# Kernel optimization log

Measured on AMD Instinct MI355X. Metric: run time of the kernel, lower is better.

## Reference

```python
import jax, jax.numpy as jnp
import numpy as np

N, D_FEAT, D, H, L = 2048, 128, 256, 8, 2
DH = D // H
E = 65536
NUM_EDGE_TYPES = 8
MAX_DIST = 10
MAX_DEGREE = 512
D_FF = 4 * D
D_OUT = 128
EPS = 1e-5


def _layernorm(x, g, b):
    mu = jnp.mean(x, axis=-1, keepdims=True)
    var = jnp.mean(jnp.square(x - mu), axis=-1, keepdims=True)
    return (x - mu) * jax.lax.rsqrt(var + EPS) * g + b


def setup_inputs() -> dict:
    key = jax.random.key(0)
    ks = jax.random.split(key, 32)
    inp = {
        "x": jax.random.normal(ks[0], (N, D_FEAT), dtype=jnp.float32),
        "edge_index": jax.random.randint(ks[1], (2, E), 0, N),
        "edge_types": jax.random.randint(ks[2], (E,), 0, NUM_EDGE_TYPES),
        "pos_encoding": jax.random.uniform(ks[3], (N, N), dtype=jnp.float32),
    }
    def xavier(k, shape):
        fan_in, fan_out = shape[0], shape[1]
        lim = float(np.sqrt(6.0 / (fan_in + fan_out)))
        return jax.random.uniform(k, shape, jnp.float32, -lim, lim)
    inp["W_emb"] = xavier(ks[4], (D_FEAT, D)); inp["b_emb"] = jnp.zeros((D,), jnp.float32)
    # stacked per-layer params, stored as [in, out] so y = x @ W + b
    inp["Wq"] = jnp.stack([xavier(jax.random.fold_in(ks[5], l), (D, D)) for l in range(L)])
    inp["Wk"] = jnp.stack([xavier(jax.random.fold_in(ks[6], l), (D, D)) for l in range(L)])
    inp["Wv"] = jnp.stack([xavier(jax.random.fold_in(ks[7], l), (D, D)) for l in range(L)])
    inp["Wo"] = jnp.stack([xavier(jax.random.fold_in(ks[8], l), (D, D)) for l in range(L)])
    for nm in ("bq", "bk", "bv", "bo"):
        inp[nm] = jnp.zeros((L, D), jnp.float32)
    inp["spd_table"] = 0.02 * jax.random.normal(ks[9], (L, MAX_DIST + 1, H), dtype=jnp.float32)
    inp["edge_table"] = 0.02 * jax.random.normal(ks[10], (L, NUM_EDGE_TYPES, H), dtype=jnp.float32)
    inp["din_emb"] = 0.02 * jax.random.normal(ks[11], (L, MAX_DEGREE + 1, D), dtype=jnp.float32)
    inp["dout_emb"] = 0.02 * jax.random.normal(ks[12], (L, MAX_DEGREE + 1, D), dtype=jnp.float32)
    inp["ln1_g"] = jnp.ones((L, D), jnp.float32); inp["ln1_b"] = jnp.zeros((L, D), jnp.float32)
    inp["ln2_g"] = jnp.ones((L, D), jnp.float32); inp["ln2_b"] = jnp.zeros((L, D), jnp.float32)
    inp["W1"] = jnp.stack([xavier(jax.random.fold_in(ks[13], l), (D, D_FF)) for l in range(L)])
    inp["b1"] = jnp.zeros((L, D_FF), jnp.float32)
    inp["W2"] = jnp.stack([xavier(jax.random.fold_in(ks[14], l), (D_FF, D)) for l in range(L)])
    inp["b2"] = jnp.zeros((L, D), jnp.float32)
    inp["W_out"] = xavier(ks[15], (D, D_OUT)); inp["b_out"] = jnp.zeros((D_OUT,), jnp.float32)
    return inp


def _forward(x, edge_index, edge_types, pos_encoding,
             W_emb, b_emb, Wq, bq, Wk, bk, Wv, bv, Wo, bo,
             spd_table, edge_table, din_emb, dout_emb,
             ln1_g, ln1_b, ln2_g, ln2_b, W1, b1, W2, b2, W_out, b_out):
    src, dst = edge_index[0], edge_index[1]
    ones = jnp.ones((E,), jnp.int32)
    deg_out = jnp.clip(jax.ops.segment_sum(ones, src, num_segments=N), 0, MAX_DEGREE)
    deg_in = jnp.clip(jax.ops.segment_sum(ones, dst, num_segments=N), 0, MAX_DEGREE)
    # SPD bucket matrix [N, N] (int), shared across layers
    spd_bucket = jnp.clip(pos_encoding[:, :N] * MAX_DIST + 0.5, 0, MAX_DIST).astype(jnp.int32)

    h = x @ W_emb + b_emb  # node embedding; dropout=0 (eval)
    scale = 1.0 / np.sqrt(DH)
    for l in range(L):
        # centrality encoding
        h = h + din_emb[l][deg_in] + dout_emb[l][deg_out]
        xn = _layernorm(h, ln1_g[l], ln1_b[l])
        q = (xn @ Wq[l] + bq[l]).reshape(N, H, DH).transpose(1, 0, 2)  # [H,N,DH]
        k = (xn @ Wk[l] + bk[l]).reshape(N, H, DH).transpose(1, 0, 2)
        v = (xn @ Wv[l] + bv[l]).reshape(N, H, DH).transpose(1, 0, 2)
        # attention bias [H, N, N]: SPD table gather + per-edge scatter-add
        bias = spd_table[l][spd_bucket].transpose(2, 0, 1)
        e_bias = edge_table[l][edge_types]  # [E, H]
        bias = bias.at[:, src, dst].add(e_bias.T)
        scores = jnp.einsum('hnd,hmd->hnm', q, k) * scale + bias
        attn = jax.nn.softmax(scores, axis=-1)
        attn_out = jnp.einsum('hnm,hmd->hnd', attn, v).transpose(1, 0, 2).reshape(N, D)
        h = h + attn_out @ Wo[l] + bo[l]
        y = _layernorm(h, ln2_g[l], ln2_b[l])
        y = jax.nn.gelu(y @ W1[l] + b1[l], approximate=False) @ W2[l] + b2[l]
        h = h + y
    return h @ W_out + b_out


def reference(x, edge_index, edge_types, pos_encoding,
              W_emb, b_emb, Wq, bq, Wk, bk, Wv, bv, Wo, bo,
              spd_table, edge_table, din_emb, dout_emb,
              ln1_g, ln1_b, ln2_g, ln2_b, W1, b1, W2, b2, W_out, b_out):
    return _forward(x, edge_index, edge_types, pos_encoding,
                    W_emb, b_emb, Wq, bq, Wk, bk, Wv, bv, Wo, bo,
                    spd_table, edge_table, din_emb, dout_emb,
                    ln1_g, ln1_b, ln2_g, ln2_b, W1, b1, W2, b2, W_out, b_out)
```

## Files before the change

kernel.cpp:

```cpp
#include <hip/hip_runtime.h>
#include <math.h>

#define N_NODES 2048
#define D_MODEL 256
#define D_FEAT 128
#define NHEAD 8
#define DH 32
#define NLAYER 2
#define NEDGE 65536
#define D_FF 1024
#define D_OUT 128
#define MAXDEG 512
#define JSPLIT 4

typedef __attribute__((ext_vector_type(8))) short short8;
typedef __attribute__((ext_vector_type(4))) float f32x4;
typedef __attribute__((ext_vector_type(4))) unsigned short u16x4;

__device__ __forceinline__ unsigned short f2bf(float f) {
    unsigned u = __float_as_uint(f);
    unsigned r = (u + 0x7FFFu + ((u >> 16) & 1u)) >> 16;
    return (unsigned short)r;
}

template <int CTRL>
__device__ __forceinline__ float dpp_ror(float x) {
    return __int_as_float(__builtin_amdgcn_update_dpp(0, __float_as_int(x), CTRL, 0xf, 0xf, false));
}

__device__ __forceinline__ void wt_tile(const float* __restrict__ W, unsigned short* __restrict__ Wt,
                                        int K, int Nc, int n0, int k0, int tid,
                                        unsigned short (*tile)[33]) {
    int r = tid >> 3, cg = (tid & 7) * 4;
    float4 w4 = *(const float4*)&W[(size_t)(k0 + r) * Nc + n0 + cg];
    tile[r][cg + 0] = f2bf(w4.x); tile[r][cg + 1] = f2bf(w4.y);
    tile[r][cg + 2] = f2bf(w4.z); tile[r][cg + 3] = f2bf(w4.w);
    __syncthreads();
    int c = tid >> 3, rg = (tid & 7) * 4;
    u16x4 o;
    #pragma unroll
    for (int j = 0; j < 4; j++) o[j] = tile[rg + j][c];
    *(u16x4*)&Wt[(size_t)(n0 + c) * K + k0 + rg] = o;
}

__global__ void mega_prep_kernel(const float* __restrict__ pos, unsigned char* __restrict__ bucket,
                                 unsigned* __restrict__ hist, int* __restrict__ deg_out,
                                 int* __restrict__ deg_in, unsigned* __restrict__ gcursor,
                                 const float* __restrict__ Wq, const float* __restrict__ Wk,
                                 const float* __restrict__ Wv, const float* __restrict__ Wo,
                                 const float* __restrict__ W1, const float* __restrict__ W2,
                                 const float* __restrict__ W_emb, const float* __restrict__ W_out,
                                 const float* __restrict__ bq, const float* __restrict__ bk,
                                 const float* __restrict__ bv,
                                 unsigned short* __restrict__ qkvt, unsigned short* __restrict__ wot,
                                 unsigned short* __restrict__ w1t, unsigned short* __restrict__ w2t,
                                 unsigned short* __restrict__ wembt, unsigned short* __restrict__ woutt,
                                 float* __restrict__ bqkv) {
    __shared__ unsigned short tile[32][33];
    int b = blockIdx.x, tid = threadIdx.x;
    if (b < 4096) {
        int i = b * 256 + tid;
        float4 p = *(const float4*)&pos[(size_t)i * 4];
        unsigned b0 = (unsigned)fminf(fmaxf(p.x * 10.f + 0.5f, 0.f), 10.f);
        unsigned b1 = (unsigned)fminf(fmaxf(p.y * 10.f + 0.5f, 0.f), 10.f);
        unsigned b2 = (unsigned)fminf(fmaxf(p.z * 10.f + 0.5f, 0.f), 10.f);
        unsigned b3 = (unsigned)fminf(fmaxf(p.w * 10.f + 0.5f, 0.f), 10.f);
        ((unsigned*)bucket)[i] = b0 | (b1 << 8) | (b2 << 16) | (b3 << 24);
        if (b < 64) {
            #pragma unroll
            for (int k = 0; k < 4; k++) hist[b * 1024 + k * 256 + tid] = 0;
        } else if (b == 64) {
            #pragma unroll
            for (int k = 0; k < 8; k++) deg_out[k * 256 + tid] = 0;
            #pragma unroll
            for (int k = 0; k < 8; k++) deg_in[k * 256 + tid] = 0;
            if (tid == 0) *gcursor = 0;
        }
        return;
    }
    int bb = b - 4096;
    if (bb < 512) {
        int z = bb >> 6, t = bb & 63;
        int l = z >> 2, which = z & 3;
        const float* W = (which == 0 ? Wq : which == 1 ? Wk : which == 2 ? Wv : Wo) + (size_t)l * 65536;
        unsigned short* dst = (which < 3) ? qkvt + (size_t)l * 196608 + which * 65536
                                          : wot + (size_t)l * 65536;
        wt_tile(W, dst, 256, 256, (t & 7) * 32, (t >> 3) * 32, tid, tile);
    } else if (bb < 1024) {
        int b2 = bb - 512, l = b2 >> 8, t = b2 & 255;
        wt_tile(W1 + (size_t)l * D_MODEL * D_FF, w1t + (size_t)l * D_MODEL * D_FF,
                D_MODEL, D_FF, (t & 31) * 32, (t >> 5) * 32, tid, tile);
    } else if (bb < 1536) {
        int b3 = bb - 1024, l = b3 >> 8, t = b3 & 255;
        wt_tile(W2 + (size_t)l * D_FF * D_MODEL, w2t + (size_t)l * D_FF * D_MODEL,
                D_FF, D_MODEL, (t & 7) * 32, (t >> 3) * 32, tid, tile);
    } else if (bb < 1568) {
        int b4 = bb - 1536;
        wt_tile(W_emb, wembt, D_FEAT, D_MODEL, (b4 & 7) * 32, (b4 >> 3) * 32, tid, tile);
    } else if (bb < 1600) {
        int b5 = bb - 1568;
        wt_tile(W_out, woutt, D_MODEL, D_OUT, (b5 & 3) * 32, (b5 >> 2) * 32, tid, tile);
    } else {
        int i = (bb - 1600) * 256 + tid;
        if (i < NLAYER * 768) {
            int l = i / 768, j = i % 768;
            const float* src = j < 256 ? bq : j < 512 ? bk : bv;
            bqkv[i] = src[l * 256 + (j & 255)];
        }
    }
}

__global__ void degree_hist_kernel(const int* __restrict__ ei,
                                   int* __restrict__ deg_out, int* __restrict__ deg_in,
                                   unsigned* __restrict__ hist) {
    int e = blockIdx.x * 256 + threadIdx.x;
    if (e < NEDGE) {
        int src = ei[e], dst = ei[NEDGE + e];
        atomicAdd(&deg_out[src], 1);
        atomicAdd(&deg_in[dst], 1);
        atomicAdd(&hist[(src >> 6) * 2048 + dst], 1);
    }
}

__global__ void edge_alloc_kernel(const unsigned* __restrict__ hist,
                                  unsigned* __restrict__ offsets, unsigned* __restrict__ cursor,
                                  unsigned* __restrict__ gend, unsigned* __restrict__ gcursor) {
    int g = blockIdx.x;
    int t = threadIdx.x;
    unsigned v = hist[g * 64 + t];
    unsigned inc = v;
    #pragma unroll
    for (int off = 1; off < 64; off <<= 1) {
        unsigned u = __shfl_up(inc, off);
        if (t >= off) inc += u;
    }
    unsigned total = __shfl(inc, 63);
    unsigned base = 0;
    if (t == 63) base = atomicAdd(gcursor, total);
    base = __shfl(base, 63);
    unsigned o = base + inc - v;
    offsets[g * 64 + t] = o;
    cursor[g * 64 + t] = o;
    if (t == 63) gend[g] = base + total;
}

__global__ void edge_scatter_kernel(const int* __restrict__ ei, const int* __restrict__ etypes,
                                    unsigned* __restrict__ cursor, unsigned* __restrict__ packed) {
    int e = blockIdx.x * 256 + threadIdx.x;
    if (e < NEDGE) {
        int src = ei[e], dst = ei[NEDGE + e];
        int key = (src >> 6) * 2048 + dst;
        unsigned pos = atomicAdd(&cursor[key], 1);
        packed[pos] = (unsigned)dst | ((unsigned)(src & 63) << 11) | ((unsigned)etypes[e] << 17);
    }
}

__global__ void centrality_ln_kernel(float* __restrict__ h,
                                     const float* __restrict__ din_l,
                                     const float* __restrict__ dout_l,
                                     const int* __restrict__ deg_in,
                                     const int* __restrict__ deg_out,
                                     const float* __restrict__ g,
                                     const float* __restrict__ b,
                                     unsigned short* __restrict__ y) {
    int row = blockIdx.x;
    int tid = threadIdx.x;
    int di = min(max(deg_in[row], 0), MAXDEG);
    int dn = min(max(deg_out[row], 0), MAXDEG);
    float v = h[row * D_MODEL + tid] + din_l[di * D_MODEL + tid] + dout_l[dn * D_MODEL + tid];
    h[row * D_MODEL + tid] = v;
    __shared__ float red[256];
    red[tid] = v; __syncthreads();
    for (int s = 128; s > 0; s >>= 1) { if (tid < s) red[tid] += red[tid + s]; __syncthreads(); }
    float mu = red[0] * (1.0f / D_MODEL);
    __syncthreads();
    float d = v - mu;
    red[tid] = d * d; __syncthreads();
    for (int s = 128; s > 0; s >>= 1) { if (tid < s) red[tid] += red[tid + s]; __syncthreads(); }
    float rstd = rsqrtf(red[0] * (1.0f / D_MODEL) + 1e-5f);
    y[row * D_MODEL + tid] = f2bf(d * rstd * g[tid] + b[tid]);
}

__global__ void layernorm_kernel(const float* __restrict__ x,
                                 const float* __restrict__ g,
                                 const float* __restrict__ b,
                                 unsigned short* __restrict__ y) {
    int row = blockIdx.x;
    int tid = threadIdx.x;
    float v = x[row * D_MODEL + tid];
    __shared__ float red[256];
    red[tid] = v; __syncthreads();
    for (int s = 128; s > 0; s >>= 1) { if (tid < s) red[tid] += red[tid + s]; __syncthreads(); }
    float mu = red[0] * (1.0f / D_MODEL);
    __syncthreads();
    float d = v - mu;
    red[tid] = d * d; __syncthreads();
    for (int s = 128; s > 0; s >>= 1) { if (tid < s) red[tid] += red[tid + s]; __syncthreads(); }
    float rstd = rsqrtf(red[0] * (1.0f / D_MODEL) + 1e-5f);
    y[row * D_MODEL + tid] = f2bf(d * rstd * g[tid] + b[tid]);
}

template <int ACT, bool RESID, bool OUTBF16, bool AFP32>
__global__ void gemm_mfma_kernel(const void* __restrict__ Av,
                                 const unsigned short* __restrict__ Wt,
                                 const float* __restrict__ bias,
                                 float* __restrict__ C, unsigned short* __restrict__ Cb,
                                 int Nc, int K) {
    __shared__ __align__(16) unsigned short As[32][72];
    __shared__ __align__(16) unsigned short Bs[64][72];
    const unsigned short* A16 = (const unsigned short*)Av;
    const float* A32 = (const float*)Av;
    int tid = threadIdx.x;
    int m0 = blockIdx.y * 32, n0 = blockIdx.x * 64;
    int w = tid >> 6, lane = tid & 63;
    int rg = (w & 1) * 16, cg = (w >> 1) * 32;
    int m = lane & 15, quad = lane >> 4;
    f32x4 acc[2] = {{0.f, 0.f, 0.f, 0.f}, {0.f, 0.f, 0.f, 0.f}};
    int ar = tid >> 3, ac = (tid & 7) * 8;
    uint4 ra; float4 fa0, fa1; uint4 rb0, rb1;
    if (AFP32) {
        fa0 = *(const float4*)&A32[(size_t)(m0 + ar) * K + ac];
        fa1 = *(const float4*)&A32[(size_t)(m0 + ar) * K + ac + 4];
    } else {
        ra = *(const uint4*)&A16[(size_t)(m0 + ar) * K + ac];
    }
    rb0 = *(const uint4*)&Wt[(size_t)(n0 + ar) * K + ac];
    rb1 = *(const uint4*)&Wt[(size_t)(n0 + 32 + ar) * K + ac];
    for (int k0 = 0; k0 < K; k0 += 64) {
        if (AFP32) {
            u16x4 t0 = {f2bf(fa0.x), f2bf(fa0.y), f2bf(fa0.z), f2bf(fa0.w)};
            u16x4 t1 = {f2bf(fa1.x), f2bf(fa1.y), f2bf(fa1.z), f2bf(fa1.w)};
            *(u16x4*)&As[ar][ac] = t0;
            *(u16x4*)&As[ar][ac + 4] = t1;
        } else {
            *(uint4*)&As[ar][ac] = ra;
        }
        *(uint4*)&Bs[ar][ac] = rb0;
        *(uint4*)&Bs[ar + 32][ac] = rb1;
        __syncthreads();
        int kn = k0 + 64;
        if (kn < K) {
            if (AFP32) {
                fa0 = *(const float4*)&A32[(size_t)(m0 + ar) * K + kn + ac];
                fa1 = *(const float4*)&A32[(size_t)(m0 + ar) * K + kn + ac + 4];
            } else {
                ra = *(const uint4*)&A16[(size_t)(m0 + ar) * K + kn + ac];
            }
            rb0 = *(const uint4*)&Wt[(size_t)(n0 + ar) * K + kn + ac];
            rb1 = *(const uint4*)&Wt[(size_t)(n0 + 32 + ar) * K + kn + ac];
        }
        #pragma unroll
        for (int ks = 0; ks < 2; ks++) {
            short8 a = *(const short8*)&As[rg + m][ks * 32 + quad * 8];
            #pragma unroll
            for (int t = 0; t < 2; t++) {
                short8 b = *(const short8*)&Bs[cg + t * 16 + m][ks * 32 + quad * 8];
                acc[t] = __builtin_amdgcn_mfma_f32_16x16x32_bf16(a, b, acc[t], 0, 0, 0);
            }
        }
        __syncthreads();
    }
    #pragma unroll
    for (int t = 0; t < 2; t++) {
        #pragma unroll
        for (int reg = 0; reg < 4; reg++) {
            int row = m0 + rg + quad * 4 + reg;
            int col = n0 + cg + t * 16 + m;
            float val = acc[t][reg] + bias[col];
            if (ACT == 1) val = val * 0.5f * (1.0f + erff(val * 0.7071067811865476f));
            size_t idx = (size_t)row * Nc + col;
            if (RESID) val += C[idx];
            if (OUTBF16) Cb[idx] = f2bf(val);
            else C[idx] = val;
        }
    }
}

__global__ void gemm_oproj_kernel(const float* __restrict__ part_O,
                                  const float* __restrict__ l_part,
                                  const unsigned short* __restrict__ Wt,
                                  const float* __restrict__ bias,
                                  float* __restrict__ C) {
    __shared__ __align__(16) unsigned short As[32][72];
    __shared__ __align__(16) unsigned short Bs[64][72];
    int tid = threadIdx.x;
    int m0 = blockIdx.y * 32, n0 = blockIdx.x * 64;
    int w = tid >> 6, lane = tid & 63;
    int rg = (w & 1) * 16, cg = (w >> 1) * 32;
    int m = lane & 15, quad = lane >> 4;
    f32x4 acc[2] = {{0.f, 0.f, 0.f, 0.f}, {0.f, 0.f, 0.f, 0.f}};
    int ar = tid >> 3, ac = (tid & 7) * 8;
    int row = m0 + ar;
    for (int k0 = 0; k0 < D_MODEL; k0 += 64) {
        int col = k0 + ac;
        int hh = col >> 5;
        float L = 0.f;
        float o[8] = {0.f, 0.f, 0.f, 0.f, 0.f, 0.f, 0.f, 0.f};
        #pragma unroll
        for (int js = 0; js < JSPLIT; js++) {
            L += l_part[((size_t)js * NHEAD + hh) * N_NODES + row];
            const float* pp = &part_O[((size_t)js * N_NODES + row) * D_MODEL + col];
            float4 p0 = *(const float4*)pp;
            float4 p1 = *(const float4*)(pp + 4);
            o[0] += p0.x; o[1] += p0.y; o[2] += p0.z; o[3] += p0.w;
            o[4] += p1.x; o[5] += p1.y; o[6] += p1.z; o[7] += p1.w;
        }
        float inv = 1.0f / L;
        u16x4 t0, t1;
        #pragma unroll
        for (int j = 0; j < 4; j++) { t0[j] = f2bf(o[j] * inv); t1[j] = f2bf(o[j + 4] * inv); }
        *(u16x4*)&As[ar][ac] = t0;
        *(u16x4*)&As[ar][ac + 4] = t1;
        *(uint4*)&Bs[ar][ac] = *(const uint4*)&Wt[(size_t)(n0 + ar) * D_MODEL + k0 + ac];
        *(uint4*)&Bs[ar + 32][ac] = *(const uint4*)&Wt[(size_t)(n0 + 32 + ar) * D_MODEL + k0 + ac];
        __syncthreads();
        #pragma unroll
        for (int ks = 0; ks < 2; ks++) {
            short8 a = *(const short8*)&As[rg + m][ks * 32 + quad * 8];
            #pragma unroll
            for (int t = 0; t < 2; t++) {
                short8 b = *(const short8*)&Bs[cg + t * 16 + m][ks * 32 + quad * 8];
                acc[t] = __builtin_amdgcn_mfma_f32_16x16x32_bf16(a, b, acc[t], 0, 0, 0);
            }
        }
        __syncthreads();
    }
    #pragma unroll
    for (int t = 0; t < 2; t++) {
        #pragma unroll
        for (int reg = 0; reg < 4; reg++) {
            int orow = m0 + rg + quad * 4 + reg;
            int ocol = n0 + cg + t * 16 + m;
            size_t idx = (size_t)orow * D_MODEL + ocol;
            C[idx] += acc[t][reg] + bias[ocol];
        }
    }
}

template <int ACT, bool VOUT>
__global__ void gemm64_kernel(const unsigned short* __restrict__ A,
                              const unsigned short* __restrict__ Wt,
                              const float* __restrict__ bias,
                              unsigned short* __restrict__ Cb,
                              unsigned short* __restrict__ vbt,
                              int Nc, int K) {
    __shared__ __align__(16) unsigned short As[64][72];
    __shared__ __align__(16) unsigned short Bs[64][72];
    int tid = threadIdx.x;
    int m0 = blockIdx.y * 64, n0 = blockIdx.x * 64;
    int w = tid >> 6, lane = tid & 63;
    int wr = (w & 1) * 32, wc = (w >> 1) * 32;
    int m = lane & 15, quad = lane >> 4;
    f32x4 acc[2][2] = {{{0.f,0.f,0.f,0.f},{0.f,0.f,0.f,0.f}},{{0.f,0.f,0.f,0.f},{0.f,0.f,0.f,0.f}}};
    int sr = tid >> 2, sg = (tid & 3) * 16;
    uint4 a0 = *(const uint4*)&A[(size_t)(m0 + sr) * K + sg];
    uint4 a1 = *(const uint4*)&A[(size_t)(m0 + sr) * K + sg + 8];
    uint4 b0 = *(const uint4*)&Wt[(size_t)(n0 + sr) * K + sg];
    uint4 b1 = *(const uint4*)&Wt[(size_t)(n0 + sr) * K + sg + 8];
    for (int k0 = 0; k0 < K; k0 += 64) {
        *(uint4*)&As[sr][sg] = a0;
        *(uint4*)&As[sr][sg + 8] = a1;
        *(uint4*)&Bs[sr][sg] = b0;
        *(uint4*)&Bs[sr][sg + 8] = b1;
        __syncthreads();
        int kn = k0 + 64;
        if (kn < K) {
            a0 = *(const uint4*)&A[(size_t)(m0 + sr) * K + kn + sg];
            a1 = *(const uint4*)&A[(size_t)(m0 + sr) * K + kn + sg + 8];
            b0 = *(const uint4*)&Wt[(size_t)(n0 + sr) * K + kn + sg];
            b1 = *(const uint4*)&Wt[(size_t)(n0 + sr) * K + kn + sg + 8];
        }
        #pragma unroll
        for (int kh = 0; kh < 2; kh++) {
            short8 x0 = *(const short8*)&As[wr + m][kh * 32 + quad * 8];
            short8 x1 = *(const short8*)&As[wr + 16 + m][kh * 32 + quad * 8];
            short8 y0 = *(const short8*)&Bs[wc + m][kh * 32 + quad * 8];
            short8 y1 = *(const short8*)&Bs[wc + 16 + m][kh * 32 + quad * 8];
            acc[0][0] = __builtin_amdgcn_mfma_f32_16x16x32_bf16(x0, y0, acc[0][0], 0, 0, 0);
            acc[0][1] = __builtin_amdgcn_mfma_f32_16x16x32_bf16(x0, y1, acc[0][1], 0, 0, 0);
            acc[1][0] = __builtin_amdgcn_mfma_f32_16x16x32_bf16(x1, y0, acc[1][0], 0, 0, 0);
            acc[1][1] = __builtin_amdgcn_mfma_f32_16x16x32_bf16(x1, y1, acc[1][1], 0, 0, 0);
        }
        __syncthreads();
    }
    if (VOUT && n0 >= 512) {
        #pragma unroll
        for (int mt = 0; mt < 2; mt++) {
            #pragma unroll
            for (int nt = 0; nt < 2; nt++) {
                int row0 = m0 + wr + mt * 16 + quad * 4;
                int col = n0 + wc + nt * 16 + m;
                float bcol = bias[col];
                u16x4 tv;
                #pragma unroll
                for (int reg = 0; reg < 4; reg++) tv[reg] = f2bf(acc[mt][nt][reg] + bcol);
                *(u16x4*)&vbt[(size_t)(col - 512) * N_NODES + row0] = tv;
            }
        }
        return;
    }
    #pragma unroll
    for (int mt = 0; mt < 2; mt++) {
        #pragma unroll
        for (int nt = 0; nt < 2; nt++) {
            #pragma unroll
            for (int reg = 0; reg < 4; reg++) {
                int row = m0 + wr + mt * 16 + quad * 4 + reg;
                int col = n0 + wc + nt * 16 + m;
                float val = acc[mt][nt][reg] + bias[col];
                if (ACT == 1) val = val * 0.5f * (1.0f + erff(val * 0.7071067811865476f));
                Cb[(size_t)row * Nc + col] = f2bf(val);
            }
        }
    }
}

__global__ __launch_bounds__(256)
void flash_attn_kernel(const unsigned short* __restrict__ qkvb,
                       const unsigned short* __restrict__ vbt,
                       const unsigned char* __restrict__ bucket,
                       const float* __restrict__ spd_l,
                       const float* __restrict__ et_l,
                       const unsigned* __restrict__ offsets,
                       const unsigned* __restrict__ gend,
                       const unsigned* __restrict__ packed,
                       float* __restrict__ part_O,
                       float* __restrict__ l_part) {
    __shared__ __align__(16) unsigned short ks[64][40];
    __shared__ __align__(16) unsigned short vs[32][72];
    __shared__ __align__(16) float ov[64][68];
    __shared__ float et[8];

    int tid = threadIdx.x;
    int rb = blockIdx.x;
    int i0 = rb * 64;
    int hh = blockIdx.y;
    int js = blockIdx.z;
    int lane = tid & 63;
    if (tid < 8) et[tid] = et_l[tid * NHEAD + hh];
    float spd_reg = spd_l[(lane < 11 ? lane : 10) * NHEAD + hh];

    int w = tid >> 6;
    int m = lane & 15, quad = lane >> 4;
    int r0 = w * 16;
    short8 aq = *(const short8*)&qkvb[(size_t)(i0 + r0 + m) * 768 + hh * DH + quad * 8];
    float l_st[4] = {0.f, 0.f, 0.f, 0.f};
    f32x4 oacc[2] = {{0.f, 0.f, 0.f, 0.f}, {0.f, 0.f, 0.f, 0.f}};
    const float scale = 0.17677669529663687f;

    int krow = tid >> 2, kcol = (tid & 3) * 8;
    int vrow = tid >> 3, vcol = (tid & 7) * 8;
    int brow = tid >> 2, bcol = (tid & 3) * 16;

    for (int jt = 0; jt < N_NODES / JSPLIT / 64; jt++) {
        int j0 = js * (N_NODES / JSPLIT) + jt * 64;
        __syncthreads();
        *(uint4*)&ks[krow][kcol] =
            *(const uint4*)&qkvb[(size_t)(j0 + krow) * 768 + 256 + hh * DH + kcol];
        *(uint4*)&vs[vrow][vcol] =
            *(const uint4*)&vbt[(size_t)(hh * DH + vrow) * N_NODES + j0 + vcol];
        {
            uint4 b16 = *(const uint4*)&bucket[(size_t)(i0 + brow) * N_NODES + j0 + bcol];
            const unsigned char* bb = (const unsigned char*)&b16;
            float fb[16];
            #pragma unroll
            for (int i = 0; i < 16; i++)
                fb[i] = __int_as_float(
                    __builtin_amdgcn_ds_bpermute(((int)bb[i]) << 2, __float_as_int(spd_reg)));
            #pragma unroll
            for (int g = 0; g < 4; g++) {
                f32x4 st = {fb[g * 4], fb[g * 4 + 1], fb[g * 4 + 2], fb[g * 4 + 3]};
                *(f32x4*)&ov[brow][bcol + g * 4] = st;
            }
        }
        __syncthreads();
        {
            unsigned key0 = (unsigned)rb * 2048 + j0;
            unsigned start = offsets[key0], end = gend[key0 >> 6];
            for (unsigned i = start + tid; i < end; i += 256) {
                unsigned p = packed[i];
                atomicAdd(&ov[(p >> 11) & 63][(p & 2047) - j0], et[(p >> 17) & 7]);
            }
        }
        __syncthreads();
        float sv[4][4];
        #pragma unroll
        for (int t = 0; t < 4; t++) {
            short8 bk8 = *(const short8*)&ks[t * 16 + m][quad * 8];
            f32x4 z = {0.f, 0.f, 0.f, 0.f};
            f32x4 sacc = __builtin_amdgcn_mfma_f32_16x16x32_bf16(aq, bk8, z, 0, 0, 0);
            #pragma unroll
            for (int r = 0; r < 4; r++)
                sv[t][r] = __expf(sacc[r] * scale + ov[r0 + quad * 4 + r][t * 16 + m]);
        }
        #pragma unroll
        for (int r = 0; r < 4; r++) {
            float ps = sv[0][r] + sv[1][r] + sv[2][r] + sv[3][r];
            ps += dpp_ror<0x121>(ps);
            ps += dpp_ror<0x122>(ps);
            ps += dpp_ror<0x124>(ps);
            ps += dpp_ror<0x128>(ps);
            l_st[r] += ps;
        }
        #pragma unroll
        for (int t = 0; t < 4; t++)
            #pragma unroll
            for (int r = 0; r < 4; r++)
                ov[r0 + quad * 4 + r][t * 16 + m] = sv[t][r];
        __builtin_amdgcn_s_waitcnt(0xC07F);
        #pragma unroll
        for (int kh = 0; kh < 2; kh++) {
            f32x4 p0 = *(const f32x4*)&ov[r0 + m][kh * 32 + quad * 8];
            f32x4 p1 = *(const f32x4*)&ov[r0 + m][kh * 32 + quad * 8 + 4];
            short8 pa;
            pa[0] = (short)f2bf(p0[0]); pa[1] = (short)f2bf(p0[1]);
            pa[2] = (short)f2bf(p0[2]); pa[3] = (short)f2bf(p0[3]);
            pa[4] = (short)f2bf(p1[0]); pa[5] = (short)f2bf(p1[1]);
            pa[6] = (short)f2bf(p1[2]); pa[7] = (short)f2bf(p1[3]);
            #pragma unroll
            for (int t = 0; t < 2; t++) {
                short8 vb = *(const short8*)&vs[t * 16 + m][kh * 32 + quad * 8];
                oacc[t] = __builtin_amdgcn_mfma_f32_16x16x32_bf16(pa, vb, oacc[t], 0, 0, 0);
            }
        }
    }
    #pragma unroll
    for (int t = 0; t < 2; t++)
        #pragma unroll
        for (int r = 0; r < 4; r++)
            part_O[((size_t)js * N_NODES + i0 + r0 + quad * 4 + r) * D_MODEL + hh * DH + t * 16 + m] =
                oacc[t][r];
    if (m == 0) {
        #pragma unroll
        for (int r = 0; r < 4; r++) {
            int row = i0 + r0 + quad * 4 + r;
            l_part[((size_t)js * NHEAD + hh) * N_NODES + row] = l_st[r];
        }
    }
}

#define WS_ALLOC(type, name, count) \
    type* name = (type*)base; base += (((size_t)(count) * sizeof(type)) + 255) & ~(size_t)255;

extern "C" void kernel_launch(void* const* d_in, const int* in_sizes, int n_in,
                              void* d_out, int out_size, void* d_ws, size_t ws_size,
                              hipStream_t stream) {
    const float* x          = (const float*)d_in[0];
    const int*   edge_index = (const int*)d_in[1];
    const int*   edge_types = (const int*)d_in[2];
    const float* pos        = (const float*)d_in[3];
    const float* W_emb      = (const float*)d_in[4];
    const float* b_emb      = (const float*)d_in[5];
    const float* Wq         = (const float*)d_in[6];
    const float* Wk         = (const float*)d_in[7];
    const float* Wv         = (const float*)d_in[8];
    const float* Wo         = (const float*)d_in[9];
    const float* bq         = (const float*)d_in[10];
    const float* bk         = (const float*)d_in[11];
    const float* bv         = (const float*)d_in[12];
    const float* bo         = (const float*)d_in[13];
    const float* spd_table  = (const float*)d_in[14];
    const float* edge_table = (const float*)d_in[15];
    const float* din_emb    = (const float*)d_in[16];
    const float* dout_emb   = (const float*)d_in[17];
    const float* ln1_g      = (const float*)d_in[18];
    const float* ln1_b      = (const float*)d_in[19];
    const float* ln2_g      = (const float*)d_in[20];
    const float* ln2_b      = (const float*)d_in[21];
    const float* W1         = (const float*)d_in[22];
    const float* b1         = (const float*)d_in[23];
    const float* W2         = (const float*)d_in[24];
    const float* b2         = (const float*)d_in[25];
    const float* W_out      = (const float*)d_in[26];
    const float* b_out      = (const float*)d_in[27];
    float* out = (float*)d_out;

    char* base = (char*)d_ws;
    WS_ALLOC(int, deg_out, N_NODES)
    WS_ALLOC(int, deg_in, N_NODES)
    WS_ALLOC(float, h, N_NODES * D_MODEL)
    WS_ALLOC(unsigned short, xb, N_NODES * D_MODEL)
    WS_ALLOC(unsigned short, qkvb, N_NODES * 768)
    WS_ALLOC(unsigned short, vbt, D_MODEL * N_NODES)
    WS_ALLOC(unsigned short, ffnb, N_NODES * D_FF)
    WS_ALLOC(unsigned char, bucket, (size_t)N_NODES * N_NODES)
    WS_ALLOC(unsigned short, qkvt, NLAYER * 768 * D_MODEL)
    WS_ALLOC(unsigned short, wot, NLAYER * D_MODEL * D_MODEL)
    WS_ALLOC(unsigned short, w1t, NLAYER * D_MODEL * D_FF)
    WS_ALLOC(unsigned short, w2t, NLAYER * D_FF * D_MODEL)
    WS_ALLOC(unsigned short, wembt, D_FEAT * D_MODEL)
    WS_ALLOC(unsigned short, woutt, D_MODEL * D_OUT)
    WS_ALLOC(float, bqkv, NLAYER * 768)
    WS_ALLOC(unsigned, hist, 65536)
    WS_ALLOC(unsigned, offsets, 65536)
    WS_ALLOC(unsigned, cursor, 65536)
    WS_ALLOC(unsigned, gend, 1024)
    WS_ALLOC(unsigned, gcursor, 1)
    WS_ALLOC(unsigned, packed, NEDGE)
    WS_ALLOC(float, part_O, (size_t)JSPLIT * N_NODES * D_MODEL)
    WS_ALLOC(float, l_part, (size_t)JSPLIT * NHEAD * N_NODES)

    mega_prep_kernel<<<5702, 256, 0, stream>>>(pos, bucket, hist, deg_out, deg_in, gcursor,
                                               Wq, Wk, Wv, Wo, W1, W2, W_emb, W_out,
                                               bq, bk, bv, qkvt, wot, w1t, w2t, wembt, woutt, bqkv);
    degree_hist_kernel<<<NEDGE / 256, 256, 0, stream>>>(edge_index, deg_out, deg_in, hist);
    edge_alloc_kernel<<<1024, 64, 0, stream>>>(hist, offsets, cursor, gend, gcursor);
    edge_scatter_kernel<<<NEDGE / 256, 256, 0, stream>>>(edge_index, edge_types, cursor, packed);

    gemm_mfma_kernel<0, false, false, true><<<dim3(D_MODEL / 64, N_NODES / 32), 256, 0, stream>>>(
        x, wembt, b_emb, h, nullptr, D_MODEL, D_FEAT);

    for (int l = 0; l < NLAYER; l++) {
        centrality_ln_kernel<<<N_NODES, 256, 0, stream>>>(
            h, din_emb + (size_t)l * (MAXDEG + 1) * D_MODEL,
            dout_emb + (size_t)l * (MAXDEG + 1) * D_MODEL, deg_in, deg_out,
            ln1_g + l * D_MODEL, ln1_b + l * D_MODEL, xb);

        gemm64_kernel<0, true><<<dim3(768 / 64, N_NODES / 64), 256, 0, stream>>>(
            xb, qkvt + (size_t)l * 768 * D_MODEL, bqkv + l * 768, qkvb, vbt, 768, D_MODEL);

        flash_attn_kernel<<<dim3(N_NODES / 64, NHEAD, JSPLIT), 256, 0, stream>>>(
            qkvb, vbt, bucket, spd_table + (size_t)l * 11 * NHEAD,
            edge_table + (size_t)l * 8 * NHEAD, offsets, gend, packed, part_O, l_part);

        gemm_oproj_kernel<<<dim3(D_MODEL / 64, N_NODES / 32), 256, 0, stream>>>(
            part_O, l_part, wot + (size_t)l * D_MODEL * D_MODEL, bo + l * D_MODEL, h);

        layernorm_kernel<<<N_NODES, 256, 0, stream>>>(h, ln2_g + l * D_MODEL, ln2_b + l * D_MODEL, xb);

        gemm64_kernel<1, false><<<dim3(D_FF / 64, N_NODES / 64), 256, 0, stream>>>(
            xb, w1t + (size_t)l * D_MODEL * D_FF, b1 + l * D_FF, ffnb, nullptr, D_FF, D_MODEL);

        gemm_mfma_kernel<0, true, false, false><<<dim3(D_MODEL / 64, N_NODES / 32), 256, 0, stream>>>(
            ffnb, w2t + (size_t)l * D_FF * D_MODEL, b2 + l * D_MODEL, h, nullptr, D_MODEL, D_FF);
    }

    gemm_mfma_kernel<0, false, false, true><<<dim3(D_OUT / 64, N_NODES / 32), 256, 0, stream>>>(
        h, woutt, b_out, out, nullptr, D_OUT, D_MODEL);
}
```

Measured before the change: 303.6 us.

## Double-buffer attention bias tile, prefetch K/V, and coalesce V-transpose stores

The flash attention loop now keeps a double-buffered float tile that holds only the per-edge bias scatter, zeroing the next buffer while the current one is consumed. K and V tiles are prefetched into registers one iteration ahead, which cuts the barriers per tile from three to two. SPD bias lookup moves into the score loop with per-element byte loads of the bucket matrix. Probabilities are staged in a separate bf16 shared buffer so conversion happens once on write. The QKV GEMM's transposed V output is staged through shared memory so global writes are 16-byte coalesced, at the cost of one extra barrier and uncoalesced byte loads for the buckets.

```diff
diff --git a/kernel.cpp b/kernel.cpp
--- a/kernel.cpp
+++ b/kernel.cpp
@@ -388,15 +388,19 @@
         for (int mt = 0; mt < 2; mt++) {
             #pragma unroll
             for (int nt = 0; nt < 2; nt++) {
-                int row0 = m0 + wr + mt * 16 + quad * 4;
-                int col = n0 + wc + nt * 16 + m;
-                float bcol = bias[col];
-                u16x4 tv;
+                int cl = wc + nt * 16 + m;
+                float bcol = bias[n0 + cl];
                 #pragma unroll
-                for (int reg = 0; reg < 4; reg++) tv[reg] = f2bf(acc[mt][nt][reg] + bcol);
-                *(u16x4*)&vbt[(size_t)(col - 512) * N_NODES + row0] = tv;
-            }
-        }
+                for (int reg = 0; reg < 4; reg++)
+                    As[cl][wr + mt * 16 + quad * 4 + reg] = f2bf(acc[mt][nt][reg] + bcol);
+            }
+        }
+        __syncthreads();
+        int rr = tid >> 2, cc = (tid & 3) * 16;
+        uint4 o0 = *(const uint4*)&As[rr][cc];
+        uint4 o1 = *(const uint4*)&As[rr][cc + 8];
+        *(uint4*)&vbt[(size_t)(n0 - 512 + rr) * N_NODES + m0 + cc] = o0;
+        *(uint4*)&vbt[(size_t)(n0 - 512 + rr) * N_NODES + m0 + cc + 8] = o1;
         return;
     }
     #pragma unroll
@@ -428,7 +432,8 @@
                        float* __restrict__ l_part) {
     __shared__ __align__(16) unsigned short ks[64][40];
     __shared__ __align__(16) unsigned short vs[32][72];
-    __shared__ __align__(16) float ov[64][68];
+    __shared__ __align__(16) unsigned short ps[64][72];
+    __shared__ __align__(16) float ov[2][64][64];
     __shared__ float et[8];
 
     int tid = threadIdx.x;
@@ -447,42 +452,44 @@
     float l_st[4] = {0.f, 0.f, 0.f, 0.f};
     f32x4 oacc[2] = {{0.f, 0.f, 0.f, 0.f}, {0.f, 0.f, 0.f, 0.f}};
     const float scale = 0.17677669529663687f;
+    const int NT = N_NODES / JSPLIT / 64;
 
     int krow = tid >> 2, kcol = (tid & 3) * 8;
     int vrow = tid >> 3, vcol = (tid & 7) * 8;
-    int brow = tid >> 2, bcol = (tid & 3) * 16;
-
-    for (int jt = 0; jt < N_NODES / JSPLIT / 64; jt++) {
-        int j0 = js * (N_NODES / JSPLIT) + jt * 64;
-        __syncthreads();
-        *(uint4*)&ks[krow][kcol] =
-            *(const uint4*)&qkvb[(size_t)(j0 + krow) * 768 + 256 + hh * DH + kcol];
-        *(uint4*)&vs[vrow][vcol] =
-            *(const uint4*)&vbt[(size_t)(hh * DH + vrow) * N_NODES + j0 + vcol];
-        {
-            uint4 b16 = *(const uint4*)&bucket[(size_t)(i0 + brow) * N_NODES + j0 + bcol];
-            const unsigned char* bb = (const unsigned char*)&b16;
-            float fb[16];
-            #pragma unroll
-            for (int i = 0; i < 16; i++)
-                fb[i] = __int_as_float(
-                    __builtin_amdgcn_ds_bpermute(((int)bb[i]) << 2, __float_as_int(spd_reg)));
-            #pragma unroll
-            for (int g = 0; g < 4; g++) {
-                f32x4 st = {fb[g * 4], fb[g * 4 + 1], fb[g * 4 + 2], fb[g * 4 + 3]};
-                *(f32x4*)&ov[brow][bcol + g * 4] = st;
-            }
-        }
-        __syncthreads();
+    int zr = tid >> 2, zc = (tid & 3) * 16;
+
+    #pragma unroll
+    for (int g = 0; g < 4; g++) *(f32x4*)&ov[0][zr][zc + g * 4] = (f32x4){0.f, 0.f, 0.f, 0.f};
+    int jbase = js * (N_NODES / JSPLIT);
+    uint4 kpre = *(const uint4*)&qkvb[(size_t)(jbase + krow) * 768 + 256 + hh * DH + kcol];
+    uint4 vpre = *(const uint4*)&vbt[(size_t)(hh * DH + vrow) * N_NODES + jbase + vcol];
+    __syncthreads();
+
+    for (int jt = 0; jt < NT; jt++) {
+        int j0 = jbase + jt * 64;
+        int p = jt & 1;
+        *(uint4*)&ks[krow][kcol] = kpre;
+        *(uint4*)&vs[vrow][vcol] = vpre;
         {
             unsigned key0 = (unsigned)rb * 2048 + j0;
             unsigned start = offsets[key0], end = gend[key0 >> 6];
             for (unsigned i = start + tid; i < end; i += 256) {
-                unsigned p = packed[i];
-                atomicAdd(&ov[(p >> 11) & 63][(p & 2047) - j0], et[(p >> 17) & 7]);
-            }
-        }
-        __syncthreads();
+                unsigned pk = packed[i];
+                atomicAdd(&ov[p][(pk >> 11) & 63][(pk & 2047) - j0], et[(pk >> 17) & 7]);
+            }
+        }
+        __syncthreads();
+        if (jt + 1 < NT) {
+            int jn = j0 + 64;
+            kpre = *(const uint4*)&qkvb[(size_t)(jn + krow) * 768 + 256 + hh * DH + kcol];
+            vpre = *(const uint4*)&vbt[(size_t)(hh * DH + vrow) * N_NODES + jn + vcol];
+        }
+        unsigned char bb[16];
+        #pragma unroll
+        for (int t = 0; t < 4; t++)
+            #pragma unroll
+            for (int r = 0; r < 4; r++)
+                bb[t * 4 + r] = bucket[(size_t)(i0 + r0 + quad * 4 + r) * N_NODES + j0 + t * 16 + m];
         float sv[4][4];
         #pragma unroll
         for (int t = 0; t < 4; t++) {
@@ -490,39 +497,42 @@
             f32x4 z = {0.f, 0.f, 0.f, 0.f};
             f32x4 sacc = __builtin_amdgcn_mfma_f32_16x16x32_bf16(aq, bk8, z, 0, 0, 0);
             #pragma unroll
+            for (int r = 0; r < 4; r++) {
+                float spdv = __int_as_float(__builtin_amdgcn_ds_bpermute(
+                    ((int)bb[t * 4 + r]) << 2, __float_as_int(spd_reg)));
+                sv[t][r] = __expf(sacc[r] * scale + spdv + ov[p][r0 + quad * 4 + r][t * 16 + m]);
+            }
+        }
+        #pragma unroll
+        for (int r = 0; r < 4; r++) {
+            float psum = sv[0][r] + sv[1][r] + sv[2][r] + sv[3][r];
+            psum += dpp_ror<0x121>(psum);
+            psum += dpp_ror<0x122>(psum);
+            psum += dpp_ror<0x124>(psum);
+            psum += dpp_ror<0x128>(psum);
+            l_st[r] += psum;
+        }
+        #pragma unroll
+        for (int t = 0; t < 4; t++)
+            #pragma unroll
             for (int r = 0; r < 4; r++)
-                sv[t][r] = __expf(sacc[r] * scale + ov[r0 + quad * 4 + r][t * 16 + m]);
-        }
-        #pragma unroll
-        for (int r = 0; r < 4; r++) {
-            float ps = sv[0][r] + sv[1][r] + sv[2][r] + sv[3][r];
-            ps += dpp_ror<0x121>(ps);
-            ps += dpp_ror<0x122>(ps);
-            ps += dpp_ror<0x124>(ps);
-            ps += dpp_ror<0x128>(ps);
-            l_st[r] += ps;
-        }
-        #pragma unroll
-        for (int t = 0; t < 4; t++)
-            #pragma unroll
-            for (int r = 0; r < 4; r++)
-                ov[r0 + quad * 4 + r][t * 16 + m] = sv[t][r];
+                ps[r0 + quad * 4 + r][t * 16 + m] = f2bf(sv[t][r]);
+        if (jt + 1 < NT) {
+            #pragma unroll
+            for (int g = 0; g < 4; g++)
+                *(f32x4*)&ov[p ^ 1][zr][zc + g * 4] = (f32x4){0.f, 0.f, 0.f, 0.f};
+        }
         __builtin_amdgcn_s_waitcnt(0xC07F);
         #pragma unroll
         for (int kh = 0; kh < 2; kh++) {
-            f32x4 p0 = *(const f32x4*)&ov[r0 + m][kh * 32 + quad * 8];
-            f32x4 p1 = *(const f32x4*)&ov[r0 + m][kh * 32 + quad * 8 + 4];
-            short8 pa;
-            pa[0] = (short)f2bf(p0[0]); pa[1] = (short)f2bf(p0[1]);
-            pa[2] = (short)f2bf(p0[2]); pa[3] = (short)f2bf(p0[3]);
-            pa[4] = (short)f2bf(p1[0]); pa[5] = (short)f2bf(p1[1]);
-            pa[6] = (short)f2bf(p1[2]); pa[7] = (short)f2bf(p1[3]);
+            short8 pa = *(const short8*)&ps[r0 + m][kh * 32 + quad * 8];
             #pragma unroll
             for (int t = 0; t < 2; t++) {
                 short8 vb = *(const short8*)&vs[t * 16 + m][kh * 32 + quad * 8];
                 oacc[t] = __builtin_amdgcn_mfma_f32_16x16x32_bf16(pa, vb, oacc[t], 0, 0, 0);
             }
         }
+        __syncthreads();
     }
     #pragma unroll
     for (int t = 0; t < 2; t++)
```

Measured after the change: 322.5 us. 6.2% more time.

## Prefetch next attention tile into registers and stage V-transpose stores through LDS

Applied to the files above, without the earlier changes.

The attention kernel now loads the next K, V and bucket tile into registers right after the tile barrier, so those global loads overlap the edge-bias atomics and MFMA work of the current tile. The barrier at the top of the loop is moved to the end of the loop body. Separately, the V-transpose epilogue of the QKV GEMM writes its results into shared memory first and then issues coalesced 16-byte row stores to vbt, replacing scattered 8-byte stores. In exchange this costs extra registers and one more barrier in the epilogue, and it reuses the As tile, which must be large enough for the transposed layout.

```diff
diff --git a/kernel.cpp b/kernel.cpp
--- a/kernel.cpp
+++ b/kernel.cpp
@@ -388,15 +388,19 @@
         for (int mt = 0; mt < 2; mt++) {
             #pragma unroll
             for (int nt = 0; nt < 2; nt++) {
-                int row0 = m0 + wr + mt * 16 + quad * 4;
-                int col = n0 + wc + nt * 16 + m;
-                float bcol = bias[col];
-                u16x4 tv;
+                int cl = wc + nt * 16 + m;
+                float bcol = bias[n0 + cl];
                 #pragma unroll
-                for (int reg = 0; reg < 4; reg++) tv[reg] = f2bf(acc[mt][nt][reg] + bcol);
-                *(u16x4*)&vbt[(size_t)(col - 512) * N_NODES + row0] = tv;
-            }
-        }
+                for (int reg = 0; reg < 4; reg++)
+                    As[cl][wr + mt * 16 + quad * 4 + reg] = f2bf(acc[mt][nt][reg] + bcol);
+            }
+        }
+        __syncthreads();
+        int rr = tid >> 2, cc = (tid & 3) * 16;
+        uint4 o0 = *(const uint4*)&As[rr][cc];
+        uint4 o1 = *(const uint4*)&As[rr][cc + 8];
+        *(uint4*)&vbt[(size_t)(n0 - 512 + rr) * N_NODES + m0 + cc] = o0;
+        *(uint4*)&vbt[(size_t)(n0 - 512 + rr) * N_NODES + m0 + cc + 8] = o1;
         return;
     }
     #pragma unroll
@@ -447,21 +451,23 @@
     float l_st[4] = {0.f, 0.f, 0.f, 0.f};
     f32x4 oacc[2] = {{0.f, 0.f, 0.f, 0.f}, {0.f, 0.f, 0.f, 0.f}};
     const float scale = 0.17677669529663687f;
+    const int NT = N_NODES / JSPLIT / 64;
 
     int krow = tid >> 2, kcol = (tid & 3) * 8;
     int vrow = tid >> 3, vcol = (tid & 7) * 8;
     int brow = tid >> 2, bcol = (tid & 3) * 16;
 
-    for (int jt = 0; jt < N_NODES / JSPLIT / 64; jt++) {
-        int j0 = js * (N_NODES / JSPLIT) + jt * 64;
-        __syncthreads();
-        *(uint4*)&ks[krow][kcol] =
-            *(const uint4*)&qkvb[(size_t)(j0 + krow) * 768 + 256 + hh * DH + kcol];
-        *(uint4*)&vs[vrow][vcol] =
-            *(const uint4*)&vbt[(size_t)(hh * DH + vrow) * N_NODES + j0 + vcol];
+    int jbase = js * (N_NODES / JSPLIT);
+    uint4 kpre = *(const uint4*)&qkvb[(size_t)(jbase + krow) * 768 + 256 + hh * DH + kcol];
+    uint4 vpre = *(const uint4*)&vbt[(size_t)(hh * DH + vrow) * N_NODES + jbase + vcol];
+    uint4 bpre = *(const uint4*)&bucket[(size_t)(i0 + brow) * N_NODES + jbase + bcol];
+
+    for (int jt = 0; jt < NT; jt++) {
+        int j0 = jbase + jt * 64;
+        *(uint4*)&ks[krow][kcol] = kpre;
+        *(uint4*)&vs[vrow][vcol] = vpre;
         {
-            uint4 b16 = *(const uint4*)&bucket[(size_t)(i0 + brow) * N_NODES + j0 + bcol];
-            const unsigned char* bb = (const unsigned char*)&b16;
+            const unsigned char* bb = (const unsigned char*)&bpre;
             float fb[16];
             #pragma unroll
             for (int i = 0; i < 16; i++)
@@ -474,6 +480,12 @@
             }
         }
         __syncthreads();
+        if (jt + 1 < NT) {
+            int jn = j0 + 64;
+            kpre = *(const uint4*)&qkvb[(size_t)(jn + krow) * 768 + 256 + hh * DH + kcol];
+            vpre = *(const uint4*)&vbt[(size_t)(hh * DH + vrow) * N_NODES + jn + vcol];
+            bpre = *(const uint4*)&bucket[(size_t)(i0 + brow) * N_NODES + jn + bcol];
+        }
         {
             unsigned key0 = (unsigned)rb * 2048 + j0;
             unsigned start = offsets[key0], end = gend[key0 >> 6];
@@ -523,6 +535,7 @@
                 oacc[t] = __builtin_amdgcn_mfma_f32_16x16x32_bf16(pa, vb, oacc[t], 0, 0, 0);
             }
         }
+        __syncthreads();
     }
     #pragma unroll
     for (int t = 0; t < 2; t++)
```

Measured after the change: 302.5 us. Within noise of the previous version (-0.3%).
